# Kernel tuning notes

Hardware: AMD Instinct MI355X
Metric: run time of the kernel (lower is better)

Reference implementation:

```python
import jax, jax.numpy as jnp
import numpy as np

NUM_HEADS = 12  # per init_kwargs


def setup_inputs() -> dict:
    key = jax.random.key(0)
    k1, k2, k3 = jax.random.split(key, 3)
    B, H, W, D = 1, 64, 64, 768
    x = jax.random.normal(k1, (B, H, W, D), dtype=jnp.float32)
    # torch nn.Linear weights are [out, in]; small init keeps softmax well-conditioned
    w_qkv = jax.random.normal(k2, (3 * D, D), dtype=jnp.float32) * 0.02
    w_proj = jax.random.normal(k3, (D, D), dtype=jnp.float32) * 0.02
    b_proj = jnp.zeros((D,), dtype=jnp.float32)
    return {"x": x, "w_qkv": w_qkv, "w_proj": w_proj, "b_proj": b_proj}


def reference(x, w_qkv, w_proj, b_proj):
    B, H, W, D = x.shape
    S = H * W
    nh = NUM_HEADS
    hd = D // nh
    scale = hd ** (-0.5)
    # qkv: [B, S, 3, nh, hd] -> q,k,v each [B, nh, S, hd]
    qkv = jnp.einsum('bhwd,ed->bhwe', x, w_qkv).reshape(B, S, 3, nh, hd)
    qkv = jnp.transpose(qkv, (2, 0, 3, 1, 4))
    q, k, v = qkv[0], qkv[1], qkv[2]
    # full O(S^2) attention matrix, as in the original module
    wei = jnp.einsum('bnqd,bnkd->bnqk', q * scale, k)
    wei = jax.nn.softmax(wei, axis=-1)
    # att_drop omitted (eval mode / deterministic baseline)
    out = jnp.einsum('bnqk,bnkd->bnqd', wei, v)  # [B, nh, S, hd]
    # [B, nh, H, W, hd] -> [B, H, W, nh*hd]
    out = jnp.transpose(out.reshape(B, nh, H, W, hd), (0, 2, 3, 1, 4)).reshape(B, H, W, D)
    proj = jnp.einsum('bhwd,ed->bhwe', out, w_proj) + b_proj
    return proj
```

## Files before the change

### kernel.cpp

```cpp
#include <hip/hip_runtime.h>
#include <hip/hip_bf16.h>
#include <math.h>

typedef short s16x8 __attribute__((ext_vector_type(8)));
typedef unsigned u32x4 __attribute__((ext_vector_type(4)));
typedef float f32x4 __attribute__((ext_vector_type(4)));
typedef float f32x16 __attribute__((ext_vector_type(16)));
typedef __hip_bfloat16 bf16;

#define GLD16(g, l)                                                        \
  __builtin_amdgcn_global_load_lds(                                        \
      (const __attribute__((address_space(1))) void*)(g),                  \
      (__attribute__((address_space(3))) void*)(l), 16, 0, 0)

#define MFMA16(a, b, c) __builtin_amdgcn_mfma_f32_16x16x32_bf16((a), (b), (c), 0, 0, 0)
#define MFMA32(a, b, c) __builtin_amdgcn_mfma_f32_32x32x16_bf16((a), (b), (c), 0, 0, 0)

static constexpr int kS = 4096;
static constexpr int kD = 768;
static constexpr int kNH = 12;
static constexpr int kHD = 64;
static constexpr int kNE = 2304;

static constexpr int kNX8 = kS * kD / 8;
static constexpr int kNWq8 = kNE * kD / 8;
static constexpr int kNWp8 = kD * kD / 8;

__global__ __launch_bounds__(256)
void k_cvt3(const float* __restrict__ x, const float* __restrict__ wq,
            const float* __restrict__ wp, bf16* __restrict__ xb,
            bf16* __restrict__ wqb, bf16* __restrict__ wpb) {
  int i = blockIdx.x * 256 + threadIdx.x;
  const float* src;
  short* dst;
  if (i < kNX8) {
    src = x; dst = (short*)xb;
  } else if (i < kNX8 + kNWq8) {
    i -= kNX8; src = wq; dst = (short*)wqb;
  } else {
    i -= kNX8 + kNWq8; if (i >= kNWp8) return;
    src = wp; dst = (short*)wpb;
  }
  const f32x4 a = *(const f32x4*)(src + i * 8);
  const f32x4 b = *(const f32x4*)(src + i * 8 + 4);
  s16x8 o;
#pragma unroll
  for (int j = 0; j < 4; ++j) {
    o[j] = (short)__bfloat16_as_ushort(__float2bfloat16(a[j]));
    o[j + 4] = (short)__bfloat16_as_ushort(__float2bfloat16(b[j]));
  }
  *(s16x8*)(dst + i * 8) = o;
}

__global__ __launch_bounds__(256, 2)
void k_qkv(const bf16* __restrict__ X, const bf16* __restrict__ W,
           bf16* __restrict__ Qw, bf16* __restrict__ Kw, bf16* __restrict__ Vw) {
  __shared__ __align__(16) short As[2][128 * 32];
  __shared__ __align__(16) short Bs[2][128 * 32];
  const int tid = threadIdx.x;
  const int wv = tid >> 6, ln = tid & 63;
  const int r = ln & 15, kq = ln >> 4;
  const int bm = blockIdx.x * 128;
  const int bn = blockIdx.y * 128;
  const int wr = wv >> 1, wc = wv & 1;
  const short* Xs = (const short*)X;
  const short* Ws = (const short*)W;

  f32x4 acc[4][4] = {};

  const int c0 = wv * 128 + ln, c1 = c0 + 64;
  const int ra0 = c0 >> 2, ka0 = c0 & 3;
  const int ra1 = c1 >> 2, ka1 = c1 & 3;
  const int off0 = wv * 1024, off1 = off0 + 512;
  const short* gA0 = Xs + (bm + ra0) * kD + ka0 * 8;
  const short* gA1 = Xs + (bm + ra1) * kD + ka1 * 8;
  const short* gB0 = Ws + (bn + ra0) * kD + ka0 * 8;
  const short* gB1 = Ws + (bn + ra1) * kD + ka1 * 8;

  GLD16(gA0, &As[0][off0]);
  GLD16(gA1, &As[0][off1]);
  GLD16(gB0, &Bs[0][off0]);
  GLD16(gB1, &Bs[0][off1]);
  __syncthreads();

  const int NT = kD / 32;
  for (int t = 0; t < NT; ++t) {
    const short* aCur = As[t & 1];
    const short* bCur = Bs[t & 1];
    if (t + 1 < NT) {
      const int k1 = (t + 1) * 32;
      short* aN = As[(t + 1) & 1];
      short* bN = Bs[(t + 1) & 1];
      GLD16(gA0 + k1, aN + off0);
      GLD16(gA1 + k1, aN + off1);
      GLD16(gB0 + k1, bN + off0);
      GLD16(gB1 + k1, bN + off1);
    }
    s16x8 a[4], b[4];
#pragma unroll
    for (int i = 0; i < 4; ++i)
      a[i] = *(const s16x8*)(aCur + (wr * 64 + i * 16 + r) * 32 + kq * 8);
#pragma unroll
    for (int j = 0; j < 4; ++j)
      b[j] = *(const s16x8*)(bCur + (wc * 64 + j * 16 + r) * 32 + kq * 8);
#pragma unroll
    for (int i = 0; i < 4; ++i)
#pragma unroll
      for (int j = 0; j < 4; ++j) acc[i][j] = MFMA16(a[i], b[j], acc[i][j]);
    __syncthreads();
  }

  const int which = bn / kD;
  bf16* dst = (which == 0) ? Qw : (which == 1) ? Kw : Vw;
  const float scl = (which == 0) ? 0.125f : 1.0f;
  const int ebase = bn - which * kD + wc * 64;
#pragma unroll
  for (int j = 0; j < 4; ++j) {
    const int e = ebase + j * 16 + r;
    const int h = e >> 6, d = e & 63;
#pragma unroll
    for (int i = 0; i < 4; ++i) {
      const int srow = bm + wr * 64 + i * 16 + kq * 4;
#pragma unroll
      for (int rr = 0; rr < 4; ++rr)
        dst[(h * kS + srow + rr) * kHD + d] = __float2bfloat16(acc[i][j][rr] * scl);
    }
  }
}

__global__ __launch_bounds__(256, 2)
void k_vt(const bf16* __restrict__ Vw, bf16* __restrict__ Vt) {
  __shared__ __align__(16) short L[64 * 72];
  const int h = blockIdx.y, st = blockIdx.x;
  const int t = threadIdx.x;
  const short* src = (const short*)Vw + (h * kS + st * 64) * kHD;
  short* dstb = (short*)Vt + h * kHD * kS;
#pragma unroll
  for (int u = 0; u < 2; ++u) {
    const int c = u * 256 + t;
    const int row = c >> 3, ch = c & 7;
    *(s16x8*)(L + row * 72 + ch * 8) = *(const s16x8*)(src + row * kHD + ch * 8);
  }
  __syncthreads();
#pragma unroll
  for (int u = 0; u < 2; ++u) {
    const int c = u * 256 + t;
    const int d = c >> 3, ch = c & 7;
    s16x8 v;
#pragma unroll
    for (int j = 0; j < 8; ++j) v[j] = L[(ch * 8 + j) * 72 + d];
    *(s16x8*)(dstb + d * kS + st * 64 + ch * 8) = v;
  }
}

__global__ __launch_bounds__(256, 3)
void k_attn(const bf16* __restrict__ Qw, const bf16* __restrict__ Kw,
            const bf16* __restrict__ Vt, bf16* __restrict__ Att) {
  __shared__ __align__(16) short Ks[3][64 * 64];
  __shared__ __align__(16) short Vs[3][64 * 64];
  const int tid = threadIdx.x;
  const int wv = tid >> 6, ln = tid & 63;
  const int qh = wv >> 1;
  const int kvh = wv & 1;
  const int col = ln & 31;
  const int lh = ln >> 5;

  const int wg = blockIdx.x;
  const int p = (wg & 7) >> 1;
  const int b = (((wg >> 3) << 1) | (wg & 1));
  const int hh = 3 * p + (b >> 6);
  const int q0 = (b & 63) * 64;

  const short* Qh = (const short*)Qw + ((size_t)hh * kS + q0 + qh * 32) * kHD;
  const short* Kh = (const short*)Kw + (size_t)hh * kS * kHD;
  const short* Vh = (const short*)Vt + (size_t)hh * kHD * kS;

  s16x8 bq[4];
#pragma unroll
  for (int kb = 0; kb < 4; ++kb)
    bq[kb] = *(const s16x8*)(Qh + col * kHD + kb * 16 + lh * 8);

  f32x16 o[2] = {};
  float lp = 0.f;

  int ldso[2];
  const short* gK[2];
  const short* gV[2];
#pragma unroll
  for (int u = 0; u < 2; ++u) {
    const int c = u * 256 + tid;
    const int kr = c >> 3, g = (c & 7) ^ (kr & 7);
    ldso[u] = c * 8;
    gK[u] = Kh + kr * kHD + g * 8;
    gV[u] = Vh + kr * kS + g * 8;
  }

  short* ksb0 = Ks[0]; short* ksb1 = Ks[1]; short* ksb2 = Ks[2];
  short* vsb0 = Vs[0]; short* vsb1 = Vs[1]; short* vsb2 = Vs[2];

#pragma unroll
  for (int t = 0; t < 3; ++t) {
    short* kd = (t == 0) ? ksb0 : (t == 1) ? ksb1 : ksb2;
    short* vd = (t == 0) ? vsb0 : (t == 1) ? vsb1 : vsb2;
#pragma unroll
    for (int u = 0; u < 2; ++u) {
      GLD16(gK[u] + t * 64 * kHD, kd + ldso[u]);
      GLD16(gV[u] + t * 64, vd + ldso[u]);
    }
  }
  asm volatile("s_waitcnt vmcnt(4)" ::: "memory");
  __builtin_amdgcn_s_barrier();

  const int krow = kvh * 32 + col;
  const int ksw = krow & 7;

  auto qk = [&](const short* ksCur) -> f32x16 {
    f32x16 z = {};
    __builtin_amdgcn_s_setprio(1);
#pragma unroll
    for (int kb = 0; kb < 4; ++kb) {
      const int ch = ((kb << 1) + lh) ^ ksw;
      s16x8 ak = *(const s16x8*)(ksCur + krow * 64 + ch * 8);
      z = MFMA32(ak, bq[kb], z);
    }
    __builtin_amdgcn_s_setprio(0);
    return z;
  };
  auto smpv = [&](const f32x16& z, const short* vsCur) {
    float pv[16];
#pragma unroll
    for (int g = 0; g < 16; ++g) {
      pv[g] = __expf(z[g]);
      lp += pv[g];
    }
    unsigned own[8], oth[8];
#pragma unroll
    for (int m = 0; m < 4; ++m) {
      own[2 * m] = (unsigned)__bfloat16_as_ushort(__float2bfloat16(pv[4 * m])) |
                   ((unsigned)__bfloat16_as_ushort(__float2bfloat16(pv[4 * m + 1])) << 16);
      own[2 * m + 1] = (unsigned)__bfloat16_as_ushort(__float2bfloat16(pv[4 * m + 2])) |
                       ((unsigned)__bfloat16_as_ushort(__float2bfloat16(pv[4 * m + 3])) << 16);
    }
#pragma unroll
    for (int i = 0; i < 8; ++i) oth[i] = __shfl_xor(own[i], 32);
    __builtin_amdgcn_s_setprio(1);
#pragma unroll
    for (int kvk = 0; kvk < 2; ++kvk) {
      u32x4 apv;
      apv[0] = lh ? oth[4 * kvk + 2] : own[4 * kvk + 0];
      apv[1] = lh ? oth[4 * kvk + 3] : own[4 * kvk + 1];
      apv[2] = lh ? own[4 * kvk + 2] : oth[4 * kvk + 0];
      apv[3] = lh ? own[4 * kvk + 3] : oth[4 * kvk + 1];
      const s16x8 ap = __builtin_bit_cast(s16x8, apv);
      const int kvg = kvh * 2 + kvk;
#pragma unroll
      for (int db = 0; db < 2; ++db) {
        const int vrow = db * 32 + col;
        const int ch = ((kvg << 1) + lh) ^ (vrow & 7);
        s16x8 vb = *(const s16x8*)(vsCur + vrow * 64 + ch * 8);
        o[db] = MFMA32(ap, vb, o[db]);
      }
    }
    __builtin_amdgcn_s_setprio(0);
  };

  const int NT = kS / 64;
  for (int kt = 0; kt < NT; kt += 2) {
    f32x16 z0 = qk(ksb0);
    f32x16 z1 = qk(ksb1);
    smpv(z0, vsb0);
    smpv(z1, vsb1);

    __builtin_amdgcn_s_barrier();

    if (kt + 3 < NT) {
      const int dk = (kt + 3) * 64 * kHD, dv = (kt + 3) * 64;
#pragma unroll
      for (int u = 0; u < 2; ++u) {
        GLD16(gK[u] + dk, ksb0 + ldso[u]);
        GLD16(gV[u] + dv, vsb0 + ldso[u]);
      }
    }
    if (kt + 4 < NT) {
      const int dk = (kt + 4) * 64 * kHD, dv = (kt + 4) * 64;
#pragma unroll
      for (int u = 0; u < 2; ++u) {
        GLD16(gK[u] + dk, ksb1 + ldso[u]);
        GLD16(gV[u] + dv, vsb1 + ldso[u]);
      }
    }
    if (kt + 4 < NT)
      asm volatile("s_waitcnt vmcnt(4)" ::: "memory");
    else
      asm volatile("s_waitcnt vmcnt(0)" ::: "memory");
    __builtin_amdgcn_s_barrier();

    short* tk = ksb2; ksb2 = ksb1; ksb1 = ksb0; ksb0 = tk;
    short* tv = vsb2; vsb2 = vsb1; vsb1 = vsb0; vsb0 = tv;
  }

  lp += __shfl_xor(lp, 32);
  float* Of = (float*)Ks;
  float* Lf = (float*)Vs;

  if (kvh == 1) {
#pragma unroll
    for (int db = 0; db < 2; ++db)
#pragma unroll
      for (int g = 0; g < 16; ++g) {
        const int qoff = (g & 3) + 8 * (g >> 2) + 4 * lh;
        Of[(qh * 32 + qoff) * 64 + db * 32 + col] = o[db][g];
      }
    if (lh == 0) Lf[qh * 32 + col] = lp;
  }
  __syncthreads();
  if (kvh == 0) {
    lp += Lf[qh * 32 + col];
    const float inv = 1.0f / lp;
    float invq[16];
#pragma unroll
    for (int g = 0; g < 16; ++g) {
      const int qoff = (g & 3) + 8 * (g >> 2) + 4 * lh;
      invq[g] = __shfl(inv, qoff);
    }
#pragma unroll
    for (int db = 0; db < 2; ++db)
#pragma unroll
      for (int g = 0; g < 16; ++g) {
        const int qoff = (g & 3) + 8 * (g >> 2) + 4 * lh;
        const int srow = q0 + qh * 32 + qoff;
        const float val =
            (o[db][g] + Of[(qh * 32 + qoff) * 64 + db * 32 + col]) * invq[g];
        Att[srow * kD + hh * kHD + db * 32 + col] = __float2bfloat16(val);
      }
  }
}

__global__ __launch_bounds__(256, 3)
void k_proj(const bf16* __restrict__ A, const bf16* __restrict__ W,
            const float* __restrict__ Bias, float* __restrict__ Out) {
  __shared__ __align__(16) short As[2][64 * 32];
  __shared__ __align__(16) short Bs[2][64 * 32];
  const int tid = threadIdx.x;
  const int wv = tid >> 6, ln = tid & 63;
  const int r = ln & 15, kq = ln >> 4;
  const int bm = blockIdx.x * 64;
  const int bn = blockIdx.y * 64;
  const int wr = wv >> 1, wc = wv & 1;
  const short* Asrc = (const short*)A;
  const short* Wsrc = (const short*)W;

  f32x4 acc[2][2] = {};
  const int c = wv * 64 + ln;
  const int ra = c >> 2, ka = c & 3;
  const int off = wv * 512;
  const short* gA = Asrc + (bm + ra) * kD + ka * 8;
  const short* gB = Wsrc + (bn + ra) * kD + ka * 8;

  GLD16(gA, &As[0][off]);
  GLD16(gB, &Bs[0][off]);
  __syncthreads();

  const int NT = kD / 32;
  for (int t = 0; t < NT; ++t) {
    const short* aCur = As[t & 1];
    const short* bCur = Bs[t & 1];
    if (t + 1 < NT) {
      const int k1 = (t + 1) * 32;
      GLD16(gA + k1, &As[(t + 1) & 1][off]);
      GLD16(gB + k1, &Bs[(t + 1) & 1][off]);
    }
    s16x8 a[2], b[2];
#pragma unroll
    for (int i = 0; i < 2; ++i)
      a[i] = *(const s16x8*)(aCur + (wr * 32 + i * 16 + r) * 32 + kq * 8);
#pragma unroll
    for (int j = 0; j < 2; ++j)
      b[j] = *(const s16x8*)(bCur + (wc * 32 + j * 16 + r) * 32 + kq * 8);
#pragma unroll
    for (int i = 0; i < 2; ++i)
#pragma unroll
      for (int j = 0; j < 2; ++j) acc[i][j] = MFMA16(a[i], b[j], acc[i][j]);
    __syncthreads();
  }
#pragma unroll
  for (int j = 0; j < 2; ++j) {
    const int e = bn + wc * 32 + j * 16 + r;
    const float bv = Bias[e];
#pragma unroll
    for (int i = 0; i < 2; ++i) {
      const int srow = bm + wr * 32 + i * 16 + kq * 4;
#pragma unroll
      for (int rr = 0; rr < 4; ++rr)
        Out[(srow + rr) * kD + e] = acc[i][j][rr] + bv;
    }
  }
}

extern "C" void kernel_launch(void* const* d_in, const int* in_sizes, int n_in,
                              void* d_out, int out_size, void* d_ws, size_t ws_size,
                              hipStream_t stream) {
  const float* x = (const float*)d_in[0];
  const float* w_qkv = (const float*)d_in[1];
  const float* w_proj = (const float*)d_in[2];
  const float* b_proj = (const float*)d_in[3];
  float* out = (float*)d_out;

  const size_t HS = (size_t)kNH * kS * kHD;
  const int nX = kS * kD;
  const int nWq = kNE * kD;
  const int nWp = kD * kD;

  bf16* Xb = (bf16*)d_ws;
  bf16* Wqb = Xb + nX;
  bf16* Wpb = Wqb + nWq;
  bf16* Qw = Wpb + nWp;
  bf16* Kw = Qw + HS;
  bf16* Vw = Kw + HS;
  bf16* Vt = Vw + HS;
  bf16* At = Vt + HS;

  const int totalC = kNX8 + kNWq8 + kNWp8;
  k_cvt3<<<(totalC + 255) / 256, 256, 0, stream>>>(x, w_qkv, w_proj, Xb, Wqb, Wpb);

  k_qkv<<<dim3(kS / 128, kNE / 128), 256, 0, stream>>>(Xb, Wqb, Qw, Kw, Vw);
  k_vt<<<dim3(kS / 64, kNH), 256, 0, stream>>>(Vw, Vt);
  k_attn<<<dim3((kS / 64) * kNH), 256, 0, stream>>>(Qw, Kw, Vt, At);
  k_proj<<<dim3(kS / 64, kD / 64), 256, 0, stream>>>(At, Wpb, b_proj, out);
}
```

Baseline: 134.5 us.

## Load K tiles directly into registers and swap lane halves with permlane32_swap

K tiles no longer go through LDS. Each wave now prefetches its 32-row K slice straight from global memory into registers, one tile ahead. Only V stays in LDS, now double-buffered as pairs of tiles, which cuts LDS use and drops the K LDS reads from the QK step. The cross-half exchange of the P fragments also switches from eight shfl_xor ops to permlane32_swap. The trade-off is more register pressure and duplicate global K reads across waves that share a KV half, which rely on cache hits.

```diff
diff --git a/kernel.cpp b/kernel.cpp
--- a/kernel.cpp
+++ b/kernel.cpp
@@ -3,6 +3,7 @@
 #include <math.h>
 
 typedef short s16x8 __attribute__((ext_vector_type(8)));
+typedef unsigned u32x2 __attribute__((ext_vector_type(2)));
 typedef unsigned u32x4 __attribute__((ext_vector_type(4)));
 typedef float f32x4 __attribute__((ext_vector_type(4)));
 typedef float f32x16 __attribute__((ext_vector_type(16)));
@@ -156,8 +157,7 @@
 __global__ __launch_bounds__(256, 3)
 void k_attn(const bf16* __restrict__ Qw, const bf16* __restrict__ Kw,
             const bf16* __restrict__ Vt, bf16* __restrict__ Att) {
-  __shared__ __align__(16) short Ks[3][64 * 64];
-  __shared__ __align__(16) short Vs[3][64 * 64];
+  __shared__ __align__(16) short Vs[2][2][64 * 64];
   const int tid = threadIdx.x;
   const int wv = tid >> 6, ln = tid & 63;
   const int qh = wv >> 1;
@@ -183,46 +183,43 @@
   f32x16 o[2] = {};
   float lp = 0.f;
 
+  const short* KhL = Kh + (kvh * 32 + col) * kHD;
+
   int ldso[2];
-  const short* gK[2];
   const short* gV[2];
 #pragma unroll
   for (int u = 0; u < 2; ++u) {
     const int c = u * 256 + tid;
     const int kr = c >> 3, g = (c & 7) ^ (kr & 7);
     ldso[u] = c * 8;
-    gK[u] = Kh + kr * kHD + g * 8;
     gV[u] = Vh + kr * kS + g * 8;
   }
 
-  short* ksb0 = Ks[0]; short* ksb1 = Ks[1]; short* ksb2 = Ks[2];
-  short* vsb0 = Vs[0]; short* vsb1 = Vs[1]; short* vsb2 = Vs[2];
-
-#pragma unroll
-  for (int t = 0; t < 3; ++t) {
-    short* kd = (t == 0) ? ksb0 : (t == 1) ? ksb1 : ksb2;
-    short* vd = (t == 0) ? vsb0 : (t == 1) ? vsb1 : vsb2;
-#pragma unroll
-    for (int u = 0; u < 2; ++u) {
-      GLD16(gK[u] + t * 64 * kHD, kd + ldso[u]);
-      GLD16(gV[u] + t * 64, vd + ldso[u]);
-    }
-  }
-  asm volatile("s_waitcnt vmcnt(4)" ::: "memory");
+#pragma unroll
+  for (int u = 0; u < 2; ++u) {
+    GLD16(gV[u] + 0 * 64, &Vs[0][0][ldso[u]]);
+    GLD16(gV[u] + 1 * 64, &Vs[0][1][ldso[u]]);
+  }
+  __builtin_amdgcn_sched_barrier(0);
+#pragma unroll
+  for (int u = 0; u < 2; ++u) {
+    GLD16(gV[u] + 2 * 64, &Vs[1][0][ldso[u]]);
+    GLD16(gV[u] + 3 * 64, &Vs[1][1][ldso[u]]);
+  }
+  s16x8 KA[4], KB[4];
+#pragma unroll
+  for (int kb = 0; kb < 4; ++kb) {
+    KA[kb] = *(const s16x8*)(KhL + 0 * 64 * kHD + (kb * 2 + lh) * 8);
+    KB[kb] = *(const s16x8*)(KhL + 1 * 64 * kHD + (kb * 2 + lh) * 8);
+  }
+  asm volatile("s_waitcnt vmcnt(12)" ::: "memory");
   __builtin_amdgcn_s_barrier();
 
-  const int krow = kvh * 32 + col;
-  const int ksw = krow & 7;
-
-  auto qk = [&](const short* ksCur) -> f32x16 {
+  auto qk = [&](const s16x8 (&K4)[4]) -> f32x16 {
     f32x16 z = {};
     __builtin_amdgcn_s_setprio(1);
 #pragma unroll
-    for (int kb = 0; kb < 4; ++kb) {
-      const int ch = ((kb << 1) + lh) ^ ksw;
-      s16x8 ak = *(const s16x8*)(ksCur + krow * 64 + ch * 8);
-      z = MFMA32(ak, bq[kb], z);
-    }
+    for (int kb = 0; kb < 4; ++kb) z = MFMA32(K4[kb], bq[kb], z);
     __builtin_amdgcn_s_setprio(0);
     return z;
   };
@@ -233,7 +230,7 @@
       pv[g] = __expf(z[g]);
       lp += pv[g];
     }
-    unsigned own[8], oth[8];
+    unsigned own[8];
 #pragma unroll
     for (int m = 0; m < 4; ++m) {
       own[2 * m] = (unsigned)__bfloat16_as_ushort(__float2bfloat16(pv[4 * m])) |
@@ -241,16 +238,16 @@
       own[2 * m + 1] = (unsigned)__bfloat16_as_ushort(__float2bfloat16(pv[4 * m + 2])) |
                        ((unsigned)__bfloat16_as_ushort(__float2bfloat16(pv[4 * m + 3])) << 16);
     }
-#pragma unroll
-    for (int i = 0; i < 8; ++i) oth[i] = __shfl_xor(own[i], 32);
     __builtin_amdgcn_s_setprio(1);
 #pragma unroll
     for (int kvk = 0; kvk < 2; ++kvk) {
+      u32x2 sA = __builtin_amdgcn_permlane32_swap(own[4 * kvk + 0], own[4 * kvk + 2], false, false);
+      u32x2 sB = __builtin_amdgcn_permlane32_swap(own[4 * kvk + 1], own[4 * kvk + 3], false, false);
       u32x4 apv;
-      apv[0] = lh ? oth[4 * kvk + 2] : own[4 * kvk + 0];
-      apv[1] = lh ? oth[4 * kvk + 3] : own[4 * kvk + 1];
-      apv[2] = lh ? own[4 * kvk + 2] : oth[4 * kvk + 0];
-      apv[3] = lh ? own[4 * kvk + 3] : oth[4 * kvk + 1];
+      apv[0] = sA[0];
+      apv[1] = sB[0];
+      apv[2] = sA[1];
+      apv[3] = sB[1];
       const s16x8 ap = __builtin_bit_cast(s16x8, apv);
       const int kvg = kvh * 2 + kvk;
 #pragma unroll
@@ -265,43 +262,43 @@
   };
 
   const int NT = kS / 64;
-  for (int kt = 0; kt < NT; kt += 2) {
-    f32x16 z0 = qk(ksb0);
-    f32x16 z1 = qk(ksb1);
-    smpv(z0, vsb0);
-    smpv(z1, vsb1);
+  for (int bi = 0; bi < NT / 2; ++bi) {
+    const int kt = 2 * bi;
+    const short* vs0 = Vs[bi & 1][0];
+    const short* vs1 = Vs[bi & 1][1];
+
+    f32x16 z0 = qk(KA);
+    if (kt + 2 < NT) {
+#pragma unroll
+      for (int kb = 0; kb < 4; ++kb)
+        KA[kb] = *(const s16x8*)(KhL + (kt + 2) * 64 * kHD + (kb * 2 + lh) * 8);
+    }
+    f32x16 z1 = qk(KB);
+    if (kt + 3 < NT) {
+#pragma unroll
+      for (int kb = 0; kb < 4; ++kb)
+        KB[kb] = *(const s16x8*)(KhL + (kt + 3) * 64 * kHD + (kb * 2 + lh) * 8);
+    }
+    smpv(z0, vs0);
+    smpv(z1, vs1);
 
     __builtin_amdgcn_s_barrier();
-
-    if (kt + 3 < NT) {
-      const int dk = (kt + 3) * 64 * kHD, dv = (kt + 3) * 64;
+    if (kt + 4 < NT) {
 #pragma unroll
       for (int u = 0; u < 2; ++u) {
-        GLD16(gK[u] + dk, ksb0 + ldso[u]);
-        GLD16(gV[u] + dv, vsb0 + ldso[u]);
+        GLD16(gV[u] + (kt + 4) * 64, &Vs[bi & 1][0][ldso[u]]);
+        GLD16(gV[u] + (kt + 5) * 64, &Vs[bi & 1][1][ldso[u]]);
       }
-    }
-    if (kt + 4 < NT) {
-      const int dk = (kt + 4) * 64 * kHD, dv = (kt + 4) * 64;
-#pragma unroll
-      for (int u = 0; u < 2; ++u) {
-        GLD16(gK[u] + dk, ksb1 + ldso[u]);
-        GLD16(gV[u] + dv, vsb1 + ldso[u]);
-      }
-    }
-    if (kt + 4 < NT)
       asm volatile("s_waitcnt vmcnt(4)" ::: "memory");
-    else
+    } else {
       asm volatile("s_waitcnt vmcnt(0)" ::: "memory");
+    }
     __builtin_amdgcn_s_barrier();
-
-    short* tk = ksb2; ksb2 = ksb1; ksb1 = ksb0; ksb0 = tk;
-    short* tv = vsb2; vsb2 = vsb1; vsb1 = vsb0; vsb0 = tv;
   }
 
   lp += __shfl_xor(lp, 32);
-  float* Of = (float*)Ks;
-  float* Lf = (float*)Vs;
+  float* Of = (float*)&Vs[0][0][0];
+  float* Lf = (float*)&Vs[1][0][0];
 
   if (kvh == 1) {
 #pragma unroll
```

After: 157.9 us. 1.17x slower.
